# Kernel optimization log

Measured on AMD Instinct MI355X. Metric: run time of the kernel, lower is better.

Reference implementation:

```python
import jax, jax.numpy as jnp
import numpy as np

N_NODES = 100000
N_EDGES = 1600000
IN_F = 256
OUT_F = 128


def setup_inputs() -> dict:
    key = jax.random.key(0)
    k_x, k_w, k_r, k_c, k_v = jax.random.split(key, 5)
    x = jax.random.normal(k_x, (N_NODES, IN_F), dtype=jnp.float32)
    weight = jax.random.normal(k_w, (IN_F, OUT_F), dtype=jnp.float32) * (1.0 / np.sqrt(IN_F))
    edge_row = jax.random.randint(k_r, (N_EDGES,), 0, N_NODES, dtype=jnp.int32)
    edge_col = jax.random.randint(k_c, (N_EDGES,), 0, N_NODES, dtype=jnp.int32)
    edge_vals = jax.random.uniform(k_v, (N_EDGES,), dtype=jnp.float32)
    return {"x": x, "weight": weight, "edge_row": edge_row,
            "edge_col": edge_col, "edge_vals": edge_vals}


def reference(x, weight, edge_row, edge_col, edge_vals):
    # Dense projection: h = x @ W  (torch: self.linear(x), bias=False)
    h = x @ weight                                   # [N, OUT_F]
    # SpMM: out[i] = sum_{(i,j) in E} A_hat[i,j] * h[j]
    messages = edge_vals[:, None] * h[edge_col]      # [E, OUT_F] gather
    out = jax.ops.segment_sum(messages, edge_row, num_segments=N_NODES)
    return out
```

## Files before the change

### kernel.cpp

```cpp
#include <hip/hip_runtime.h>
#include <hip/hip_bf16.h>


#define IN_F  256
#define OUT_F 128

typedef __attribute__((ext_vector_type(8))) short sh8;
typedef __attribute__((ext_vector_type(4))) float f32x4;

__device__ __forceinline__ unsigned short f2bf(float f) {
    unsigned u = __float_as_uint(f);
    unsigned r = u + 0x7fff + ((u >> 16) & 1);
    return (unsigned short)(r >> 16);
}
__device__ __forceinline__ float bf2f(unsigned short s) {
    return __uint_as_float(((unsigned)s) << 16);
}

__global__ __launch_bounds__(256) void wt_prep_kernel(
    const float* __restrict__ w, unsigned short* __restrict__ wt) {
    int i = blockIdx.x * 256 + threadIdx.x;
    int k = i >> 7, n = i & 127;
    wt[n * IN_F + k] = f2bf(w[i]);
}

__global__ __launch_bounds__(256) void fused_gemm_rank_kernel(
    const float* __restrict__ x, const unsigned short* __restrict__ wt,
    unsigned short* __restrict__ h, int n_nodes,
    const int* __restrict__ erow, int* __restrict__ counts,
    unsigned char* __restrict__ rank, int n_edges, int rank_blocks) {
    int g = blockIdx.x;
    int third = g / 3;
    int tid = threadIdx.x;

    if (g % 3 == 0) {
        int wv = tid >> 6, l = tid & 63;
        int l16 = l & 15, lk = (l >> 4) * 8;
        long row0 = (long)third * 128 + wv * 32;

        long rmax = n_nodes - 1;
        long ra0 = row0 + l16;      if (ra0 > rmax) ra0 = rmax;
        long ra1 = row0 + 16 + l16; if (ra1 > rmax) ra1 = rmax;
        const float* xp0 = x + ra0 * IN_F + lk;
        const float* xp1 = x + ra1 * IN_F + lk;
        const unsigned short* wp = wt + l16 * IN_F + lk;

        f32x4 acc[2][8];
        #pragma unroll
        for (int rt = 0; rt < 2; rt++)
            #pragma unroll
            for (int nt = 0; nt < 8; nt++)
                acc[rt][nt] = (f32x4){0.f, 0.f, 0.f, 0.f};

        #pragma unroll
        for (int ks = 0; ks < 8; ks++) {
            int k0 = ks * 32;
            float4 t0 = *(const float4*)(xp0 + k0);
            float4 t1 = *(const float4*)(xp0 + k0 + 4);
            float4 t2 = *(const float4*)(xp1 + k0);
            float4 t3 = *(const float4*)(xp1 + k0 + 4);
            sh8 a0, a1;
            a0[0] = (short)f2bf(t0.x); a0[1] = (short)f2bf(t0.y);
            a0[2] = (short)f2bf(t0.z); a0[3] = (short)f2bf(t0.w);
            a0[4] = (short)f2bf(t1.x); a0[5] = (short)f2bf(t1.y);
            a0[6] = (short)f2bf(t1.z); a0[7] = (short)f2bf(t1.w);
            a1[0] = (short)f2bf(t2.x); a1[1] = (short)f2bf(t2.y);
            a1[2] = (short)f2bf(t2.z); a1[3] = (short)f2bf(t2.w);
            a1[4] = (short)f2bf(t3.x); a1[5] = (short)f2bf(t3.y);
            a1[6] = (short)f2bf(t3.z); a1[7] = (short)f2bf(t3.w);
            #pragma unroll
            for (int nt = 0; nt < 8; nt++) {
                sh8 b = *(const sh8*)(wp + nt * 16 * IN_F + k0);
                acc[0][nt] = __builtin_amdgcn_mfma_f32_16x16x32_bf16(
                    a0, b, acc[0][nt], 0, 0, 0);
                acc[1][nt] = __builtin_amdgcn_mfma_f32_16x16x32_bf16(
                    a1, b, acc[1][nt], 0, 0, 0);
            }
        }

        int rbase = (l >> 4) * 4;
        #pragma unroll
        for (int rt = 0; rt < 2; rt++) {
            #pragma unroll
            for (int j = 0; j < 4; j++) {
                long r = row0 + rt * 16 + rbase + j;
                if (r < n_nodes) {
                    unsigned short* hp = h + r * OUT_F + l16;
                    #pragma unroll
                    for (int nt = 0; nt < 8; nt++)
                        hp[nt * 16] = f2bf(acc[rt][nt][j]);
                }
            }
        }
    } else {
        int rb = g - third - 1;
        int stride = rank_blocks * 256;
        int n4 = n_edges >> 2;
        for (int i = rb * 256 + tid; i < n4; i += stride) {
            int4 r = ((const int4*)erow)[i];
            uchar4 k;
            k.x = (unsigned char)atomicAdd(&counts[r.x], 1);
            k.y = (unsigned char)atomicAdd(&counts[r.y], 1);
            k.z = (unsigned char)atomicAdd(&counts[r.z], 1);
            k.w = (unsigned char)atomicAdd(&counts[r.w], 1);
            ((uchar4*)rank)[i] = k;
        }
        for (int i = (n4 << 2) + rb * 256 + tid; i < n_edges; i += stride)
            rank[i] = (unsigned char)atomicAdd(&counts[erow[i]], 1);
    }
}

__global__ __launch_bounds__(256) void scan1_kernel(
    const int* __restrict__ counts, int* __restrict__ excl,
    int* __restrict__ partials, int n) {
    __shared__ int s[256];
    int tid = threadIdx.x;
    int i = blockIdx.x * 256 + tid;
    int v = (i < n) ? counts[i] : 0;
    s[tid] = v;
    __syncthreads();
    for (int off = 1; off < 256; off <<= 1) {
        int t = (tid >= off) ? s[tid - off] : 0;
        __syncthreads();
        s[tid] += t;
        __syncthreads();
    }
    if (i < n) excl[i] = s[tid] - v;
    if (tid == 255) partials[blockIdx.x] = s[255];
}

__global__ __launch_bounds__(512) void scan2_kernel(int* partials, int nb) {
    __shared__ int s[512];
    int tid = threadIdx.x;
    int v = (tid < nb) ? partials[tid] : 0;
    s[tid] = v;
    __syncthreads();
    for (int off = 1; off < 512; off <<= 1) {
        int t = (tid >= off) ? s[tid - off] : 0;
        __syncthreads();
        s[tid] += t;
        __syncthreads();
    }
    if (tid < nb) partials[tid] = s[tid] - v;
}

__global__ __launch_bounds__(256) void scan3_kernel(
    int* __restrict__ excl, const int* __restrict__ partials, int n) {
    int i = blockIdx.x * 256 + threadIdx.x;
    if (i < n) excl[i] += partials[blockIdx.x];
}

__device__ __forceinline__ unsigned pack_edge(float v, int c) {
    unsigned q = (unsigned)__builtin_fmaf(v, 32767.f, 0.5f);
    return (q << 17) | (unsigned)c;
}

__global__ __launch_bounds__(256) void scatter_kernel(
    const int* __restrict__ erow, const int* __restrict__ ecol,
    const float* __restrict__ eval, const unsigned char* __restrict__ rank,
    const int* __restrict__ offs, unsigned* __restrict__ epack,
    int n_edges) {
    int stride = gridDim.x * 256;
    int n4 = n_edges >> 2;
    for (int i = blockIdx.x * 256 + threadIdx.x; i < n4; i += stride) {
        int4   r = ((const int4*)erow)[i];
        int4   c = ((const int4*)ecol)[i];
        float4 v = ((const float4*)eval)[i];
        uchar4 k = ((const uchar4*)rank)[i];
        epack[offs[r.x] + k.x] = pack_edge(v.x, c.x);
        epack[offs[r.y] + k.y] = pack_edge(v.y, c.y);
        epack[offs[r.z] + k.z] = pack_edge(v.z, c.z);
        epack[offs[r.w] + k.w] = pack_edge(v.w, c.w);
    }
    for (int i = (n4 << 2) + blockIdx.x * 256 + threadIdx.x; i < n_edges;
         i += stride) {
        epack[offs[erow[i]] + rank[i]] = pack_edge(eval[i], ecol[i]);
    }
}

__global__ __launch_bounds__(256) void rowsum_kernel(
    const unsigned short* __restrict__ h, const int* __restrict__ offs,
    const unsigned* __restrict__ epack,
    float* __restrict__ out, int n_nodes, int n_edges) {
    int wid = (blockIdx.x * 256 + threadIdx.x) >> 6;
    int lane = threadIdx.x & 63;
    if (wid >= n_nodes) return;

    int s = offs[wid];
    int e = (wid + 1 < n_nodes) ? offs[wid + 1] : n_edges;
    int cnt = e - s;

    const float dq = 1.0f / 32767.f;
    float a0 = 0.f, a1 = 0.f;
    for (int base = 0; base < cnt; base += 64) {
        int m = min(64, cnt - base);
        unsigned pk = 0;
        if (base + lane < cnt) pk = epack[s + base + lane];

        int j = 0;
        for (; j + 4 <= m; j += 4) {
            unsigned p0 = __shfl(pk, j);
            unsigned p1 = __shfl(pk, j + 1);
            unsigned p2 = __shfl(pk, j + 2);
            unsigned p3 = __shfl(pk, j + 3);
            unsigned hv0 = *((const unsigned*)(h + (long)(p0 & 0x1ffffu) * OUT_F) + lane);
            unsigned hv1 = *((const unsigned*)(h + (long)(p1 & 0x1ffffu) * OUT_F) + lane);
            unsigned hv2 = *((const unsigned*)(h + (long)(p2 & 0x1ffffu) * OUT_F) + lane);
            unsigned hv3 = *((const unsigned*)(h + (long)(p3 & 0x1ffffu) * OUT_F) + lane);
            float v0 = (float)(p0 >> 17) * dq;
            float v1 = (float)(p1 >> 17) * dq;
            float v2 = (float)(p2 >> 17) * dq;
            float v3 = (float)(p3 >> 17) * dq;
            a0 += v0 * bf2f((unsigned short)(hv0 & 0xffff));
            a1 += v0 * bf2f((unsigned short)(hv0 >> 16));
            a0 += v1 * bf2f((unsigned short)(hv1 & 0xffff));
            a1 += v1 * bf2f((unsigned short)(hv1 >> 16));
            a0 += v2 * bf2f((unsigned short)(hv2 & 0xffff));
            a1 += v2 * bf2f((unsigned short)(hv2 >> 16));
            a0 += v3 * bf2f((unsigned short)(hv3 & 0xffff));
            a1 += v3 * bf2f((unsigned short)(hv3 >> 16));
        }
        for (; j < m; j++) {
            unsigned p0 = __shfl(pk, j);
            unsigned hv0 = *((const unsigned*)(h + (long)(p0 & 0x1ffffu) * OUT_F) + lane);
            float v0 = (float)(p0 >> 17) * dq;
            a0 += v0 * bf2f((unsigned short)(hv0 & 0xffff));
            a1 += v0 * bf2f((unsigned short)(hv0 >> 16));
        }
    }
    float2 o; o.x = a0; o.y = a1;
    *(float2*)(out + (long)wid * OUT_F + lane * 2) = o;
}

extern "C" void kernel_launch(void* const* d_in, const int* in_sizes, int n_in,
                              void* d_out, int out_size, void* d_ws, size_t ws_size,
                              hipStream_t stream) {
    const float* x    = (const float*)d_in[0];
    const float* w    = (const float*)d_in[1];
    const int*   erow = (const int*)d_in[2];
    const int*   ecol = (const int*)d_in[3];
    const float* eval = (const float*)d_in[4];
    float* out = (float*)d_out;

    int n_nodes = in_sizes[0] / IN_F;
    int n_edges = in_sizes[2];
    int nb = (n_nodes + 255) / 256;
    int n4 = n_edges >> 2;
    int eblk = (n4 + 255) / 256;

    char* p = (char*)d_ws;
    auto alloc = [&](size_t bytes) {
        char* q = p;
        p += (bytes + 255) & ~(size_t)255;
        return q;
    };
    unsigned short* h  = (unsigned short*)alloc((size_t)n_nodes * OUT_F * 2);
    int*   counts   = (int*)alloc((size_t)n_nodes * 4);
    int*   offs     = (int*)alloc((size_t)n_nodes * 4);
    int*   partials = (int*)alloc((size_t)nb * 4);
    unsigned* epack = (unsigned*)alloc((size_t)n_edges * 4);
    unsigned char* rank = (unsigned char*)alloc((size_t)n_edges);
    unsigned short* wt  = (unsigned short*)alloc((size_t)IN_F * OUT_F * 2);

    hipMemsetAsync(counts, 0, (size_t)n_nodes * 4, stream);

    wt_prep_kernel<<<dim3((IN_F * OUT_F) / 256), 256, 0, stream>>>(w, wt);

    int gemm_blocks = (n_nodes + 127) / 128;
    int rank_blocks = eblk;
    int total_blocks = gemm_blocks + rank_blocks;
    fused_gemm_rank_kernel<<<dim3(total_blocks), 256, 0, stream>>>(
        x, wt, h, n_nodes, erow, counts, rank, n_edges, rank_blocks);

    scan1_kernel<<<dim3(nb), 256, 0, stream>>>(counts, offs, partials, n_nodes);
    scan2_kernel<<<dim3(1), 512, 0, stream>>>(partials, nb);
    scan3_kernel<<<dim3(nb), 256, 0, stream>>>(offs, partials, n_nodes);
    scatter_kernel<<<dim3(eblk), 256, 0, stream>>>(erow, ecol, eval, rank,
                                                   offs, epack, n_edges);

    rowsum_kernel<<<dim3(((long)n_nodes * 64 + 255) / 256), 256, 0, stream>>>(
        h, offs, epack, out, n_nodes, n_edges);
}
```

Measured before the change: 196.3 us.

## Rebalance fused GEMM/rank kernel and process four rows per wave in rowsum

```diff
diff --git a/kernel.cpp b/kernel.cpp
--- a/kernel.cpp
+++ b/kernel.cpp
@@ -30,83 +30,87 @@
     const int* __restrict__ erow, int* __restrict__ counts,
     unsigned char* __restrict__ rank, int n_edges, int rank_blocks) {
     int g = blockIdx.x;
-    int third = g / 3;
     int tid = threadIdx.x;
 
-    if (g % 3 == 0) {
+    if (g < rank_blocks) {
+        int stride = rank_blocks * 256;
+        int n16 = n_edges >> 4;
+        const int4* e4 = (const int4*)erow;
+        for (int t = g * 256 + tid; t < n16; t += stride) {
+            int4 r0 = e4[t * 4 + 0];
+            int4 r1 = e4[t * 4 + 1];
+            int4 r2 = e4[t * 4 + 2];
+            int4 r3 = e4[t * 4 + 3];
+            unsigned k00 = atomicAdd(&counts[r0.x], 1);
+            unsigned k01 = atomicAdd(&counts[r0.y], 1);
+            unsigned k02 = atomicAdd(&counts[r0.z], 1);
+            unsigned k03 = atomicAdd(&counts[r0.w], 1);
+            unsigned k10 = atomicAdd(&counts[r1.x], 1);
+            unsigned k11 = atomicAdd(&counts[r1.y], 1);
+            unsigned k12 = atomicAdd(&counts[r1.z], 1);
+            unsigned k13 = atomicAdd(&counts[r1.w], 1);
+            unsigned k20 = atomicAdd(&counts[r2.x], 1);
+            unsigned k21 = atomicAdd(&counts[r2.y], 1);
+            unsigned k22 = atomicAdd(&counts[r2.z], 1);
+            unsigned k23 = atomicAdd(&counts[r2.w], 1);
+            unsigned k30 = atomicAdd(&counts[r3.x], 1);
+            unsigned k31 = atomicAdd(&counts[r3.y], 1);
+            unsigned k32 = atomicAdd(&counts[r3.z], 1);
+            unsigned k33 = atomicAdd(&counts[r3.w], 1);
+            uint4 kk;
+            kk.x = (k00 & 0xff) | ((k01 & 0xff) << 8) | ((k02 & 0xff) << 16) | (k03 << 24);
+            kk.y = (k10 & 0xff) | ((k11 & 0xff) << 8) | ((k12 & 0xff) << 16) | (k13 << 24);
+            kk.z = (k20 & 0xff) | ((k21 & 0xff) << 8) | ((k22 & 0xff) << 16) | (k23 << 24);
+            kk.w = (k30 & 0xff) | ((k31 & 0xff) << 8) | ((k32 & 0xff) << 16) | (k33 << 24);
+            ((uint4*)rank)[t] = kk;
+        }
+        for (int i = (n16 << 4) + g * 256 + tid; i < n_edges; i += stride)
+            rank[i] = (unsigned char)atomicAdd(&counts[erow[i]], 1);
+    } else {
+        int gb = g - rank_blocks;
         int wv = tid >> 6, l = tid & 63;
         int l16 = l & 15, lk = (l >> 4) * 8;
-        long row0 = (long)third * 128 + wv * 32;
+        long row0 = (long)gb * 64 + wv * 16;
 
         long rmax = n_nodes - 1;
-        long ra0 = row0 + l16;      if (ra0 > rmax) ra0 = rmax;
-        long ra1 = row0 + 16 + l16; if (ra1 > rmax) ra1 = rmax;
+        long ra0 = row0 + l16; if (ra0 > rmax) ra0 = rmax;
         const float* xp0 = x + ra0 * IN_F + lk;
-        const float* xp1 = x + ra1 * IN_F + lk;
         const unsigned short* wp = wt + l16 * IN_F + lk;
 
-        f32x4 acc[2][8];
+        f32x4 acc[8];
         #pragma unroll
-        for (int rt = 0; rt < 2; rt++)
-            #pragma unroll
-            for (int nt = 0; nt < 8; nt++)
-                acc[rt][nt] = (f32x4){0.f, 0.f, 0.f, 0.f};
+        for (int nt = 0; nt < 8; nt++)
+            acc[nt] = (f32x4){0.f, 0.f, 0.f, 0.f};
 
         #pragma unroll
         for (int ks = 0; ks < 8; ks++) {
             int k0 = ks * 32;
             float4 t0 = *(const float4*)(xp0 + k0);
             float4 t1 = *(const float4*)(xp0 + k0 + 4);
-            float4 t2 = *(const float4*)(xp1 + k0);
-            float4 t3 = *(const float4*)(xp1 + k0 + 4);
-            sh8 a0, a1;
+            sh8 a0;
             a0[0] = (short)f2bf(t0.x); a0[1] = (short)f2bf(t0.y);
             a0[2] = (short)f2bf(t0.z); a0[3] = (short)f2bf(t0.w);
             a0[4] = (short)f2bf(t1.x); a0[5] = (short)f2bf(t1.y);
             a0[6] = (short)f2bf(t1.z); a0[7] = (short)f2bf(t1.w);
-            a1[0] = (short)f2bf(t2.x); a1[1] = (short)f2bf(t2.y);
-            a1[2] = (short)f2bf(t2.z); a1[3] = (short)f2bf(t2.w);
-            a1[4] = (short)f2bf(t3.x); a1[5] = (short)f2bf(t3.y);
-            a1[6] = (short)f2bf(t3.z); a1[7] = (short)f2bf(t3.w);
             #pragma unroll
             for (int nt = 0; nt < 8; nt++) {
                 sh8 b = *(const sh8*)(wp + nt * 16 * IN_F + k0);
-                acc[0][nt] = __builtin_amdgcn_mfma_f32_16x16x32_bf16(
-                    a0, b, acc[0][nt], 0, 0, 0);
-                acc[1][nt] = __builtin_amdgcn_mfma_f32_16x16x32_bf16(
-                    a1, b, acc[1][nt], 0, 0, 0);
+                acc[nt] = __builtin_amdgcn_mfma_f32_16x16x32_bf16(
+                    a0, b, acc[nt], 0, 0, 0);
             }
         }
 
         int rbase = (l >> 4) * 4;
         #pragma unroll
-        for (int rt = 0; rt < 2; rt++) {
-            #pragma unroll
-            for (int j = 0; j < 4; j++) {
-                long r = row0 + rt * 16 + rbase + j;
-                if (r < n_nodes) {
-                    unsigned short* hp = h + r * OUT_F + l16;
-                    #pragma unroll
-                    for (int nt = 0; nt < 8; nt++)
-                        hp[nt * 16] = f2bf(acc[rt][nt][j]);
-                }
-            }
-        }
-    } else {
-        int rb = g - third - 1;
-        int stride = rank_blocks * 256;
-        int n4 = n_edges >> 2;
-        for (int i = rb * 256 + tid; i < n4; i += stride) {
-            int4 r = ((const int4*)erow)[i];
-            uchar4 k;
-            k.x = (unsigned char)atomicAdd(&counts[r.x], 1);
-            k.y = (unsigned char)atomicAdd(&counts[r.y], 1);
-            k.z = (unsigned char)atomicAdd(&counts[r.z], 1);
-            k.w = (unsigned char)atomicAdd(&counts[r.w], 1);
-            ((uchar4*)rank)[i] = k;
-        }
-        for (int i = (n4 << 2) + rb * 256 + tid; i < n_edges; i += stride)
-            rank[i] = (unsigned char)atomicAdd(&counts[erow[i]], 1);
+        for (int j = 0; j < 4; j++) {
+            long r = row0 + rbase + j;
+            if (r < n_nodes) {
+                unsigned short* hp = h + r * OUT_F + l16;
+                #pragma unroll
+                for (int nt = 0; nt < 8; nt++)
+                    hp[nt * 16] = f2bf(acc[nt][j]);
+            }
+        }
     }
 }
 
@@ -184,52 +188,63 @@
     float* __restrict__ out, int n_nodes, int n_edges) {
     int wid = (blockIdx.x * 256 + threadIdx.x) >> 6;
     int lane = threadIdx.x & 63;
-    if (wid >= n_nodes) return;
-
-    int s = offs[wid];
-    int e = (wid + 1 < n_nodes) ? offs[wid + 1] : n_edges;
-    int cnt = e - s;
+    long r0 = (long)wid * 4;
+    if (r0 >= n_nodes) return;
 
     const float dq = 1.0f / 32767.f;
-    float a0 = 0.f, a1 = 0.f;
-    for (int base = 0; base < cnt; base += 64) {
-        int m = min(64, cnt - base);
-        unsigned pk = 0;
-        if (base + lane < cnt) pk = epack[s + base + lane];
-
-        int j = 0;
-        for (; j + 4 <= m; j += 4) {
-            unsigned p0 = __shfl(pk, j);
-            unsigned p1 = __shfl(pk, j + 1);
-            unsigned p2 = __shfl(pk, j + 2);
-            unsigned p3 = __shfl(pk, j + 3);
-            unsigned hv0 = *((const unsigned*)(h + (long)(p0 & 0x1ffffu) * OUT_F) + lane);
-            unsigned hv1 = *((const unsigned*)(h + (long)(p1 & 0x1ffffu) * OUT_F) + lane);
-            unsigned hv2 = *((const unsigned*)(h + (long)(p2 & 0x1ffffu) * OUT_F) + lane);
-            unsigned hv3 = *((const unsigned*)(h + (long)(p3 & 0x1ffffu) * OUT_F) + lane);
-            float v0 = (float)(p0 >> 17) * dq;
-            float v1 = (float)(p1 >> 17) * dq;
-            float v2 = (float)(p2 >> 17) * dq;
-            float v3 = (float)(p3 >> 17) * dq;
-            a0 += v0 * bf2f((unsigned short)(hv0 & 0xffff));
-            a1 += v0 * bf2f((unsigned short)(hv0 >> 16));
-            a0 += v1 * bf2f((unsigned short)(hv1 & 0xffff));
-            a1 += v1 * bf2f((unsigned short)(hv1 >> 16));
-            a0 += v2 * bf2f((unsigned short)(hv2 & 0xffff));
-            a1 += v2 * bf2f((unsigned short)(hv2 >> 16));
-            a0 += v3 * bf2f((unsigned short)(hv3 & 0xffff));
-            a1 += v3 * bf2f((unsigned short)(hv3 >> 16));
-        }
-        for (; j < m; j++) {
-            unsigned p0 = __shfl(pk, j);
-            unsigned hv0 = *((const unsigned*)(h + (long)(p0 & 0x1ffffu) * OUT_F) + lane);
-            float v0 = (float)(p0 >> 17) * dq;
-            a0 += v0 * bf2f((unsigned short)(hv0 & 0xffff));
-            a1 += v0 * bf2f((unsigned short)(hv0 >> 16));
-        }
-    }
-    float2 o; o.x = a0; o.y = a1;
-    *(float2*)(out + (long)wid * OUT_F + lane * 2) = o;
+    int wstart = -(1 << 30);
+    unsigned pk = 0;
+
+    for (int rr = 0; rr < 4; rr++) {
+        long row = r0 + rr;
+        if (row >= n_nodes) break;
+        int rs = offs[row];
+        int re = (row + 1 < n_nodes) ? offs[row + 1] : n_edges;
+
+        float a0 = 0.f, a1 = 0.f;
+        int p = rs;
+        while (p < re) {
+            if (p >= wstart + 64) {
+                wstart = p;
+                int idx = wstart + lane;
+                pk = (idx < n_edges) ? epack[idx] : 0;
+            }
+            int lim = min(re, wstart + 64);
+            for (; p + 4 <= lim; p += 4) {
+                int j = p - wstart;
+                unsigned p0 = __shfl(pk, j);
+                unsigned p1 = __shfl(pk, j + 1);
+                unsigned p2 = __shfl(pk, j + 2);
+                unsigned p3 = __shfl(pk, j + 3);
+                unsigned hv0 = *((const unsigned*)(h + (long)(p0 & 0x1ffffu) * OUT_F) + lane);
+                unsigned hv1 = *((const unsigned*)(h + (long)(p1 & 0x1ffffu) * OUT_F) + lane);
+                unsigned hv2 = *((const unsigned*)(h + (long)(p2 & 0x1ffffu) * OUT_F) + lane);
+                unsigned hv3 = *((const unsigned*)(h + (long)(p3 & 0x1ffffu) * OUT_F) + lane);
+                float v0 = (float)(p0 >> 17) * dq;
+                float v1 = (float)(p1 >> 17) * dq;
+                float v2 = (float)(p2 >> 17) * dq;
+                float v3 = (float)(p3 >> 17) * dq;
+                a0 += v0 * bf2f((unsigned short)(hv0 & 0xffff));
+                a1 += v0 * bf2f((unsigned short)(hv0 >> 16));
+                a0 += v1 * bf2f((unsigned short)(hv1 & 0xffff));
+                a1 += v1 * bf2f((unsigned short)(hv1 >> 16));
+                a0 += v2 * bf2f((unsigned short)(hv2 & 0xffff));
+                a1 += v2 * bf2f((unsigned short)(hv2 >> 16));
+                a0 += v3 * bf2f((unsigned short)(hv3 & 0xffff));
+                a1 += v3 * bf2f((unsigned short)(hv3 >> 16));
+            }
+            for (; p < lim; p++) {
+                int j = p - wstart;
+                unsigned p0 = __shfl(pk, j);
+                unsigned hv0 = *((const unsigned*)(h + (long)(p0 & 0x1ffffu) * OUT_F) + lane);
+                float v0 = (float)(p0 >> 17) * dq;
+                a0 += v0 * bf2f((unsigned short)(hv0 & 0xffff));
+                a1 += v0 * bf2f((unsigned short)(hv0 >> 16));
+            }
+        }
+        float2 o; o.x = a0; o.y = a1;
+        *(float2*)(out + row * OUT_F + lane * 2) = o;
+    }
 }
 
 extern "C" void kernel_launch(void* const* d_in, const int* in_sizes, int n_in,
@@ -245,8 +260,7 @@
     int n_nodes = in_sizes[0] / IN_F;
     int n_edges = in_sizes[2];
     int nb = (n_nodes + 255) / 256;
-    int n4 = n_edges >> 2;
-    int eblk = (n4 + 255) / 256;
+    int eblk = ((n_edges >> 2) + 255) / 256;
 
     char* p = (char*)d_ws;
     auto alloc = [&](size_t bytes) {
@@ -266,10 +280,9 @@
 
     wt_prep_kernel<<<dim3((IN_F * OUT_F) / 256), 256, 0, stream>>>(w, wt);
 
-    int gemm_blocks = (n_nodes + 127) / 128;
-    int rank_blocks = eblk;
-    int total_blocks = gemm_blocks + rank_blocks;
-    fused_gemm_rank_kernel<<<dim3(total_blocks), 256, 0, stream>>>(
+    int rank_blocks = (n_edges + 256 * 16 - 1) / (256 * 16);
+    int gemm_blocks = (n_nodes + 63) / 64;
+    fused_gemm_rank_kernel<<<dim3(rank_blocks + gemm_blocks), 256, 0, stream>>>(
         x, wt, h, n_nodes, erow, counts, rank, n_edges, rank_blocks);
 
     scan1_kernel<<<dim3(nb), 256, 0, stream>>>(counts, offs, partials, n_nodes);
@@ -278,6 +291,7 @@
     scatter_kernel<<<dim3(eblk), 256, 0, stream>>>(erow, ecol, eval, rank,
                                                    offs, epack, n_edges);
 
-    rowsum_kernel<<<dim3(((long)n_nodes * 64 + 255) / 256), 256, 0, stream>>>(
+    long waves = ((long)n_nodes + 3) / 4;
+    rowsum_kernel<<<dim3((waves * 64 + 255) / 256), 256, 0, stream>>>(
         h, offs, epack, out, n_nodes, n_edges);
 }
```

After: 227.9 us. 1.16x slower.
